# Optimization experiments

Measured on AMD Instinct MI355X. Metric: run time of the kernel, lower is better.

Reference implementation:

```python
import jax, jax.numpy as jnp
import numpy as np

V, E, H, B, T, O = 100000, 300, 512, 512, 64, 2


def setup_inputs() -> dict:
    key = jax.random.key(0)
    ks = jax.random.split(key, 12)
    bound = 1.0 / np.sqrt(H)
    u = lambda k, shape: jax.random.uniform(k, shape, jnp.float32, -bound, bound)
    tokens = jax.random.randint(ks[0], (B, T), 0, V)  # int token ids
    emb = jax.random.normal(ks[1], (V, E), jnp.float32) * 0.05  # pretrained embeddings
    # GRU params stacked over 2 directions: [2, 3H, in], [2, 3H, H], [2, 3H]
    w_ih0 = u(ks[2], (2, 3 * H, E))
    w_hh0 = u(ks[3], (2, 3 * H, H))
    b_ih0 = u(ks[4], (2, 3 * H))
    b_hh0 = u(ks[5], (2, 3 * H))
    w_ih1 = u(ks[6], (2, 3 * H, 2 * H))
    w_hh1 = u(ks[7], (2, 3 * H, H))
    b_ih1 = u(ks[8], (2, 3 * H))
    b_hh1 = u(ks[9], (2, 3 * H))
    fc_w = u(ks[10], (O, 2 * H))
    fc_b = u(ks[11], (O,))
    return dict(tokens=tokens, emb=emb, w_ih0=w_ih0, w_hh0=w_hh0, b_ih0=b_ih0,
                b_hh0=b_hh0, w_ih1=w_ih1, w_hh1=w_hh1, b_ih1=b_ih1, b_hh1=b_hh1,
                fc_w=fc_w, fc_b=fc_b)


def _gru_dir(x, Wih, Whh, bih, bhh):
    # x: [B, T, in] -> [B, T, H]; PyTorch GRU cell math.
    gx = jnp.einsum('bti,gi->btg', x, Wih) + bih  # input gates precomputed [B,T,3H]
    h_units = Whh.shape[1]

    def step(h, g):
        gh = h @ Whh.T + bhh
        xr, xz, xn = jnp.split(g, 3, axis=-1)
        hr, hz, hn = jnp.split(gh, 3, axis=-1)
        r = jax.nn.sigmoid(xr + hr)
        z = jax.nn.sigmoid(xz + hz)
        n = jnp.tanh(xn + r * hn)
        h_new = (1.0 - z) * n + z * h
        return h_new, h_new

    h0 = jnp.zeros((x.shape[0], h_units), x.dtype)
    _, ys = jax.lax.scan(step, h0, jnp.swapaxes(gx, 0, 1))  # scan over time
    return jnp.swapaxes(ys, 0, 1)


def _gru_bidir(x, w_ih, w_hh, b_ih, b_hh):
    fwd = _gru_dir(x, w_ih[0], w_hh[0], b_ih[0], b_hh[0])
    bwd = _gru_dir(x[:, ::-1], w_ih[1], w_hh[1], b_ih[1], b_hh[1])[:, ::-1]
    return jnp.concatenate([fwd, bwd], axis=-1)  # [B, T, 2H]


def reference(tokens, emb, w_ih0, w_hh0, b_ih0, b_hh0, w_ih1, w_hh1, b_ih1,
              b_hh1, fc_w, fc_b):
    x = emb[tokens]                                   # [B, T, E]
    h1 = _gru_bidir(x, w_ih0, w_hh0, b_ih0, b_hh0)    # [B, T, 2H]
    h2 = _gru_bidir(h1, w_ih1, w_hh1, b_ih1, b_hh1)   # [B, T, 2H]
    # dropout output is discarded in the original forward (out = output[:, -1, :])
    last = h2[:, -1, :]                               # [B, 2H]
    return last @ fc_w.T + fc_b                       # [B, O]
```

## Files before the change

kernel.cpp:

```cpp
#include <hip/hip_runtime.h>
#include <stdint.h>


#define NTW 192
#define MTX 2048

typedef _Float16 half8 __attribute__((ext_vector_type(8)));
typedef _Float16 half4_t __attribute__((ext_vector_type(4)));
typedef float float4_t __attribute__((ext_vector_type(4)));

__device__ __forceinline__ void gl_lds16(const void* g, void* l) {
  __builtin_amdgcn_global_load_lds(
      (const __attribute__((address_space(1))) void*)g,
      (__attribute__((address_space(3))) void*)l, 16, 0, 0);
}

__device__ __forceinline__ float sigm_f(float x) { return 1.f / (1.f + __expf(-x)); }
__device__ __forceinline__ float tanh_f(float x) { return 1.f - 2.f / (__expf(2.f * x) + 1.f); }

__global__ void pack_b_kernel(const float* __restrict__ src, _Float16* __restrict__ dst,
                              int K, int KI) {
  int gid = blockIdx.x * 256 + threadIdx.x;
  int l = gid & 63, unit = gid >> 6;
  int nt = unit / KI, ks = unit - nt * KI;
  if (nt >= NTW) return;
  int row = nt * 16 + (l & 15);
  int col0 = ks * 32 + ((l >> 4) << 3);
  half8 v;
#pragma unroll
  for (int j = 0; j < 8; ++j) {
    int c = col0 + j;
    v[j] = (c < K) ? (_Float16)src[(long)row * K + c] : (_Float16)0.f;
  }
  *(half8*)(dst + (long)unit * 512 + l * 8) = v;
}

__global__ void gather_kernel(const int* __restrict__ tokens, const float* __restrict__ emb,
                              _Float16* __restrict__ x0) {
  int gid = blockIdx.x * 256 + threadIdx.x;
  int l = gid & 63, unit = gid >> 6;
  int mt = unit / 10, ks = unit - mt * 10;
  if (mt >= MTX) return;
  int row = mt * 16 + (l & 15);
  const float* e = emb + (long)tokens[row] * 300;
  int col0 = ks * 32 + ((l >> 4) << 3);
  half8 v;
#pragma unroll
  for (int j = 0; j < 8; ++j) {
    int c = col0 + j;
    v[j] = (c < 300) ? (_Float16)e[c] : (_Float16)0.f;
  }
  *(half8*)(x0 + (long)unit * 512 + l * 8) = v;
}

__global__ __launch_bounds__(256) void gemm_bt_kernel(
    const _Float16* __restrict__ A, const _Float16* __restrict__ Bw,
    const float* __restrict__ bias, _Float16* __restrict__ C, int KI) {
  __shared__ _Float16 As[8 * 512];
  __shared__ _Float16 Bs[8 * 512];
  const int bx = blockIdx.x, by = blockIdx.y;
  const int tid = threadIdx.x, w = tid >> 6, l = tid & 63;
  const int wm = w >> 1, wn = w & 1, ln = l & 15;
  const int mt0 = by * 8, nt0 = bx * 8;
  float4_t acc[4][4];
#pragma unroll
  for (int i = 0; i < 4; ++i)
#pragma unroll
    for (int j = 0; j < 4; ++j) acc[i][j] = 0.f;
  for (int it = 0; it < KI; ++it) {
    __syncthreads();
    gl_lds16(A + ((long)(mt0 + w) * KI + it) * 512 + l * 8, As + w * 512 + l * 8);
    gl_lds16(A + ((long)(mt0 + w + 4) * KI + it) * 512 + l * 8, As + (w + 4) * 512 + l * 8);
    gl_lds16(Bw + ((long)(nt0 + w) * KI + it) * 512 + l * 8, Bs + w * 512 + l * 8);
    gl_lds16(Bw + ((long)(nt0 + w + 4) * KI + it) * 512 + l * 8, Bs + (w + 4) * 512 + l * 8);
    __syncthreads();
    half8 af[4], bf[4];
#pragma unroll
    for (int i = 0; i < 4; ++i) af[i] = *(const half8*)(As + (wm * 4 + i) * 512 + l * 8);
#pragma unroll
    for (int j = 0; j < 4; ++j) bf[j] = *(const half8*)(Bs + (wn * 4 + j) * 512 + l * 8);
#pragma unroll
    for (int i = 0; i < 4; ++i)
#pragma unroll
      for (int j = 0; j < 4; ++j)
        acc[i][j] = __builtin_amdgcn_mfma_f32_16x16x32_f16(af[i], bf[j], acc[i][j], 0, 0, 0);
  }
#pragma unroll
  for (int i = 0; i < 4; ++i)
#pragma unroll
    for (int j = 0; j < 4; ++j) {
      int mt = mt0 + wm * 4 + i, ntile = nt0 + wn * 4 + j;
      float bv = bias[ntile * 16 + ln];
      half4_t o;
#pragma unroll
      for (int r = 0; r < 4; ++r) o[r] = (_Float16)(acc[i][j][r] + bv);
      *(half4_t*)(C + ((long)mt * NTW + ntile) * 256 + l * 4) = o;
    }
}

__global__ __launch_bounds__(256, 1) void gru_scan_kernel(
    const _Float16* __restrict__ whh,
    const float* __restrict__ bhh,
    const _Float16* __restrict__ gx,
    _Float16* hbuf, _Float16* ys,
    float* last,
    unsigned int* cnt) {
  __shared__ alignas(16) _Float16 hs[32 * 512];
  __shared__ alignas(16) _Float16 hx[4 * 512];
  const int bid = blockIdx.x;
  const int d = bid >> 7, mtg = (bid >> 3) & 15, ntb = bid & 7;
  const int tid = threadIdx.x, w = tid >> 6, l = tid & 63;
  const int lq = l >> 4, ln = l & 15;
  unsigned int* flags = cnt + (d * 16 + mtg) * 16;
  const int hcol = ntb * 64 + w * 16 + ln;

  half8 bf[3][16];
#pragma unroll
  for (int g = 0; g < 3; ++g) {
    const int tg = d * 96 + g * 32 + ntb * 4 + w;
#pragma unroll
    for (int ks = 0; ks < 16; ++ks)
      bf[g][ks] = *(const half8*)(whh + (long)(tg * 16 + ks) * 512 + l * 8);
  }
  const float bh0 = bhh[d * 1536 + hcol];
  const float bh1 = bhh[d * 1536 + 512 + hcol];
  const float bh2 = bhh[d * 1536 + 1024 + hcol];
  float hreg[2][4] = {{0.f, 0.f, 0.f, 0.f}, {0.f, 0.f, 0.f, 0.f}};
  const int mtr0 = mtg * 2;
  const int ntg0 = d * 96 + ntb * 4 + w;
  const unsigned long long* hb8 = (const unsigned long long*)hbuf;
  unsigned long long* lds64 = (unsigned long long*)hs;

  float xr[2][4], xz[2][4], xn[2][4];
  auto load_gx = [&](int step, float (&vr)[2][4], float (&vz)[2][4], float (&vn)[2][4]) {
    const int t2 = d ? (63 - step) : step;
    const int rm2 = t2 & 15, tq2 = t2 >> 4;
    const int eoff2 = ((rm2 >> 2) * 16 + ln) * 4 + (rm2 & 3);
#pragma unroll
    for (int i = 0; i < 2; ++i)
#pragma unroll
      for (int r = 0; r < 4; ++r) {
        const int b = (mtr0 + i) * 16 + lq * 4 + r;
        const long gbase = ((long)(b * 4 + tq2) * 192 + ntg0) * 256 + eoff2;
        vr[i][r] = (float)gx[gbase];
        vz[i][r] = (float)gx[gbase + 32 * 256];
        vn[i][r] = (float)gx[gbase + 64 * 256];
      }
  };
  load_gx(0, xr, xz, xn);

  for (int s = 0; s < 64; ++s) {
    const int par = s & 1;
    const int t_in = d ? (63 - s) : s;
    const int rm = t_in & 15, tq = t_in >> 4;

    {
      const unsigned long long* src =
          hb8 + (long)(d * 2 + par) * 65536 + (long)mtg * 4096;
#pragma unroll
      for (int rr = 0; rr < 2; ++rr) {
        unsigned long long t0[8];
#pragma unroll
        for (int j = 0; j < 4; ++j) {
          const int f = (rr * 4 + j) * 256 + tid;
          t0[j * 2] = __hip_atomic_load(src + (long)f * 2, __ATOMIC_RELAXED,
                                        __HIP_MEMORY_SCOPE_AGENT);
          t0[j * 2 + 1] = __hip_atomic_load(src + (long)f * 2 + 1, __ATOMIC_RELAXED,
                                            __HIP_MEMORY_SCOPE_AGENT);
        }
#pragma unroll
        for (int j = 0; j < 4; ++j) {
          const int f = (rr * 4 + j) * 256 + tid;
          lds64[f * 2] = t0[j * 2];
          lds64[f * 2 + 1] = t0[j * 2 + 1];
        }
      }
    }
    __syncthreads();

    float4_t acc[3][2];
#pragma unroll
    for (int g = 0; g < 3; ++g) { acc[g][0] = 0.f; acc[g][1] = 0.f; }
#pragma unroll
    for (int kk = 0; kk < 2; ++kk) {
      half8 af[2][8];
#pragma unroll
      for (int i = 0; i < 2; ++i)
#pragma unroll
        for (int k2 = 0; k2 < 8; ++k2)
          af[i][k2] = *(const half8*)(hs + (i * 16 + kk * 8 + k2) * 512 + l * 8);
#pragma unroll
      for (int k2 = 0; k2 < 8; ++k2)
#pragma unroll
        for (int i = 0; i < 2; ++i)
#pragma unroll
          for (int g = 0; g < 3; ++g)
            acc[g][i] = __builtin_amdgcn_mfma_f32_16x16x32_f16(af[i][k2], bf[g][kk * 8 + k2],
                                                               acc[g][i], 0, 0, 0);
    }

#pragma unroll
    for (int i = 0; i < 2; ++i) {
      const int mtile_i = mtr0 + i;
#pragma unroll
      for (int r = 0; r < 4; ++r) {
        const int b = mtile_i * 16 + lq * 4 + r;
        const long gmt = (long)b * 4 + tq;
        const float rg = sigm_f(xr[i][r] + acc[0][i][r] + bh0);
        const float zg = sigm_f(xz[i][r] + acc[1][i][r] + bh1);
        const float ng = tanh_f(xn[i][r] + rg * (acc[2][i][r] + bh2));
        const float hv = (1.f - zg) * ng + zg * hreg[i][r];
        hreg[i][r] = hv;
        hx[(i * 2 + (w >> 1)) * 512 + (((w & 1) * 2 + (ln >> 3)) * 16 + lq * 4 + r) * 8 +
           (ln & 7)] = (_Float16)hv;
        if (ys != nullptr) {
          const int kcol = d * 512 + hcol;
          ys[(gmt * 32 + (kcol >> 5)) * 512 + (((kcol >> 3) & 3) * 16 + rm) * 8 + (kcol & 7)] =
              (_Float16)hv;
        }
        if (last != nullptr && ((d == 0 && s == 63) || (d == 1 && s == 0)))
          last[(long)b * 1024 + d * 512 + hcol] = hv;
      }
    }
    if (s == 63) break;

    __syncthreads();
    {
      const int u = tid >> 6, lw = tid & 63;
      union { half8 h; unsigned long long q[2]; } wb;
      wb.h = *(const half8*)(hx + u * 512 + lw * 8);
      unsigned long long* dst = (unsigned long long*)hbuf +
                                (long)(d * 2 + (par ^ 1)) * 65536 +
                                ((long)((mtg * 2 + (u >> 1)) * 16 + ntb * 2 + (u & 1))) * 128 +
                                lw * 2;
      __hip_atomic_store(dst, wb.q[0], __ATOMIC_RELAXED, __HIP_MEMORY_SCOPE_AGENT);
      __hip_atomic_store(dst + 1, wb.q[1], __ATOMIC_RELAXED, __HIP_MEMORY_SCOPE_AGENT);
    }
    __syncthreads();

    if (tid == 0)
      __hip_atomic_store(flags + ntb, (unsigned int)(s + 1), __ATOMIC_RELAXED,
                         __HIP_MEMORY_SCOPE_AGENT);

    load_gx(s + 1, xr, xz, xn);

    {
      const unsigned int tgt = (unsigned int)(s + 1);
      long guard = 0;
      for (;;) {
        const unsigned int f = __hip_atomic_load(flags + (l & 7), __ATOMIC_RELAXED,
                                                 __HIP_MEMORY_SCOPE_AGENT);
        if (__all((int)(f >= tgt))) break;
        __builtin_amdgcn_s_sleep(1);
        if (++guard > (1L << 24)) break;
      }
      __builtin_amdgcn_fence(__ATOMIC_ACQUIRE, "workgroup");
    }
  }
}

__global__ void fc_kernel(const float* __restrict__ lastb, const float* __restrict__ fw,
                          const float* __restrict__ fb, float* __restrict__ out) {
  const int b = blockIdx.x, l = threadIdx.x;
  const float* x = lastb + (long)b * 1024;
  float a0 = 0.f, a1 = 0.f;
  for (int k = l; k < 1024; k += 64) {
    const float v = x[k];
    a0 += v * fw[k];
    a1 += v * fw[1024 + k];
  }
#pragma unroll
  for (int off = 32; off > 0; off >>= 1) {
    a0 += __shfl_down(a0, off, 64);
    a1 += __shfl_down(a1, off, 64);
  }
  if (l == 0) {
    out[b * 2 + 0] = a0 + fb[0];
    out[b * 2 + 1] = a1 + fb[1];
  }
}

extern "C" void kernel_launch(void* const* d_in, const int* in_sizes, int n_in,
                              void* d_out, int out_size, void* d_ws, size_t ws_size,
                              hipStream_t stream) {
  const int* tokens = (const int*)d_in[0];
  const float* emb = (const float*)d_in[1];
  const float* w_ih0 = (const float*)d_in[2];
  const float* w_hh0 = (const float*)d_in[3];
  const float* b_ih0 = (const float*)d_in[4];
  const float* b_hh0 = (const float*)d_in[5];
  const float* w_ih1 = (const float*)d_in[6];
  const float* w_hh1 = (const float*)d_in[7];
  const float* b_ih1 = (const float*)d_in[8];
  const float* b_hh1 = (const float*)d_in[9];
  const float* fc_w = (const float*)d_in[10];
  const float* fc_b = (const float*)d_in[11];
  float* out = (float*)d_out;

  char* ws = (char*)d_ws;
  size_t off = 0;
  auto alloc = [&](size_t bytes) -> void* {
    void* p = ws + off;
    off += (bytes + 255) & ~(size_t)255;
    return p;
  };
  _Float16* W0f = (_Float16*)alloc(192L * 10 * 512 * 2);
  _Float16* W1f = (_Float16*)alloc(192L * 32 * 512 * 2);
  _Float16* Wh0f = (_Float16*)alloc(192L * 16 * 512 * 2);
  _Float16* Wh1f = (_Float16*)alloc(192L * 16 * 512 * 2);
  _Float16* x0f = (_Float16*)alloc(2048L * 10 * 512 * 2);
  _Float16* x1f = (_Float16*)alloc(2048L * 32 * 512 * 2);
  _Float16* gxb = (_Float16*)alloc(2048L * 192 * 256 * 2);
  char* hz = ws + off;
  _Float16* hbuf = (_Float16*)alloc(4L * 32 * 8192 * 2);
  unsigned int* cnt = (unsigned int*)alloc(4096);
  const size_t hz_bytes = 4L * 32 * 8192 * 2 + 4096;
  float* lastb = (float*)alloc(512L * 1024 * 4);
  if (off > ws_size) return;

  pack_b_kernel<<<dim3(192 * 10 * 64 / 256), 256, 0, stream>>>(w_ih0, W0f, 300, 10);
  pack_b_kernel<<<dim3(192 * 32 * 64 / 256), 256, 0, stream>>>(w_ih1, W1f, 1024, 32);
  pack_b_kernel<<<dim3(192 * 16 * 64 / 256), 256, 0, stream>>>(w_hh0, Wh0f, 512, 16);
  pack_b_kernel<<<dim3(192 * 16 * 64 / 256), 256, 0, stream>>>(w_hh1, Wh1f, 512, 16);
  gather_kernel<<<dim3(2048 * 10 * 64 / 256), 256, 0, stream>>>(tokens, emb, x0f);

  gemm_bt_kernel<<<dim3(24, 256), 256, 0, stream>>>(x0f, W0f, b_ih0, gxb, 10);
  hipMemsetAsync(hz, 0, hz_bytes, stream);
  gru_scan_kernel<<<dim3(256), 256, 0, stream>>>(Wh0f, b_hh0, gxb, hbuf, x1f, nullptr, cnt);

  gemm_bt_kernel<<<dim3(24, 256), 256, 0, stream>>>(x1f, W1f, b_ih1, gxb, 32);
  hipMemsetAsync(hz, 0, hz_bytes, stream);
  gru_scan_kernel<<<dim3(256), 256, 0, stream>>>(Wh1f, b_hh1, gxb, hbuf, nullptr, lastb, cnt);

  fc_kernel<<<dim3(512), 64, 0, stream>>>(lastb, fc_w, fc_b, out);
}
```

Measured before the change: 1.264 ms.

## Split each block's two row tiles into staggered halves with separate flags

Each scan block now handles its two 16-row batch tiles as separate A and B halves, each with its own LDS buffer and completion flag array. Tile A's hidden state is published and flagged before tile B's MFMA and gate math run, so peers waiting on A can proceed earlier. The flag polling also moves to the start of each step, just before the loads, rather than sitting after publication. The aim is to overlap cross-block synchronisation latency with the other tile's compute, at the cost of more barriers and twice as many flag polls per step. It also assumes the flag buffer is sized for 32 row groups per direction instead of 16.

```diff
diff --git a/kernel.cpp b/kernel.cpp
--- a/kernel.cpp
+++ b/kernel.cpp
@@ -105,13 +105,16 @@
     _Float16* hbuf, _Float16* ys,
     float* last,
     unsigned int* cnt) {
-  __shared__ alignas(16) _Float16 hs[32 * 512];
-  __shared__ alignas(16) _Float16 hx[4 * 512];
+  __shared__ alignas(16) _Float16 hsA[16 * 512];
+  __shared__ alignas(16) _Float16 hsB[16 * 512];
+  __shared__ alignas(16) _Float16 hx[2 * 512];
   const int bid = blockIdx.x;
-  const int d = bid >> 7, mtg = (bid >> 3) & 15, ntb = bid & 7;
+  const int d = bid >> 7, mp = (bid >> 3) & 15, ntb = bid & 7;
+  const int rA = mp * 2, rB = rA + 1;
   const int tid = threadIdx.x, w = tid >> 6, l = tid & 63;
   const int lq = l >> 4, ln = l & 15;
-  unsigned int* flags = cnt + (d * 16 + mtg) * 16;
+  unsigned int* flagsA = cnt + (d * 32 + rA) * 16;
+  unsigned int* flagsB = cnt + (d * 32 + rB) * 16;
   const int hcol = ntb * 64 + w * 16 + ln;
 
   half8 bf[3][16];
@@ -125,137 +128,166 @@
   const float bh0 = bhh[d * 1536 + hcol];
   const float bh1 = bhh[d * 1536 + 512 + hcol];
   const float bh2 = bhh[d * 1536 + 1024 + hcol];
-  float hreg[2][4] = {{0.f, 0.f, 0.f, 0.f}, {0.f, 0.f, 0.f, 0.f}};
-  const int mtr0 = mtg * 2;
+  float hrA[4] = {0.f, 0.f, 0.f, 0.f};
+  float hrB[4] = {0.f, 0.f, 0.f, 0.f};
   const int ntg0 = d * 96 + ntb * 4 + w;
   const unsigned long long* hb8 = (const unsigned long long*)hbuf;
-  unsigned long long* lds64 = (unsigned long long*)hs;
-
-  float xr[2][4], xz[2][4], xn[2][4];
-  auto load_gx = [&](int step, float (&vr)[2][4], float (&vz)[2][4], float (&vn)[2][4]) {
+  unsigned long long* hb8w = (unsigned long long*)hbuf;
+  unsigned long long* lA64 = (unsigned long long*)hsA;
+  unsigned long long* lB64 = (unsigned long long*)hsB;
+  const unsigned long long* hx64 = (const unsigned long long*)hx;
+
+  float xrA[4], xzA[4], xnA[4], xrB[4], xzB[4], xnB[4];
+  auto load_gx = [&](int step, int rc, float (&vr)[4], float (&vz)[4], float (&vn)[4]) {
     const int t2 = d ? (63 - step) : step;
     const int rm2 = t2 & 15, tq2 = t2 >> 4;
     const int eoff2 = ((rm2 >> 2) * 16 + ln) * 4 + (rm2 & 3);
 #pragma unroll
-    for (int i = 0; i < 2; ++i)
-#pragma unroll
-      for (int r = 0; r < 4; ++r) {
-        const int b = (mtr0 + i) * 16 + lq * 4 + r;
-        const long gbase = ((long)(b * 4 + tq2) * 192 + ntg0) * 256 + eoff2;
-        vr[i][r] = (float)gx[gbase];
-        vz[i][r] = (float)gx[gbase + 32 * 256];
-        vn[i][r] = (float)gx[gbase + 64 * 256];
-      }
+    for (int r = 0; r < 4; ++r) {
+      const int b = rc * 16 + lq * 4 + r;
+      const long gbase = ((long)(b * 4 + tq2) * 192 + ntg0) * 256 + eoff2;
+      vr[r] = (float)gx[gbase];
+      vz[r] = (float)gx[gbase + 32 * 256];
+      vn[r] = (float)gx[gbase + 64 * 256];
+    }
   };
-  load_gx(0, xr, xz, xn);
+  load_gx(0, rA, xrA, xzA, xnA);
+  load_gx(0, rB, xrB, xzB, xnB);
+
+  auto poll = [&](unsigned int* flags, unsigned int tgt) {
+    long guard = 0;
+    for (;;) {
+      const unsigned int f = __hip_atomic_load(flags + (l & 7), __ATOMIC_RELAXED,
+                                               __HIP_MEMORY_SCOPE_AGENT);
+      if (__all((int)(f >= tgt))) break;
+      __builtin_amdgcn_s_sleep(1);
+      if (++guard > (1L << 24)) break;
+    }
+  };
 
   for (int s = 0; s < 64; ++s) {
     const int par = s & 1;
     const int t_in = d ? (63 - s) : s;
     const int rm = t_in & 15, tq = t_in >> 4;
-
+    const unsigned long long* src = hb8 + (long)(d * 2 + par) * 65536;
+
+    poll(flagsA, (unsigned int)s);
+    poll(flagsB, (unsigned int)s);
+    __builtin_amdgcn_fence(__ATOMIC_ACQUIRE, "workgroup");
+    unsigned long long ta[8], tb[8];
+#pragma unroll
+    for (int j = 0; j < 8; ++j)
+      ta[j] = __hip_atomic_load(src + (long)rA * 2048 + j * 256 + tid, __ATOMIC_RELAXED,
+                                __HIP_MEMORY_SCOPE_AGENT);
+#pragma unroll
+    for (int j = 0; j < 8; ++j)
+      tb[j] = __hip_atomic_load(src + (long)rB * 2048 + j * 256 + tid, __ATOMIC_RELAXED,
+                                __HIP_MEMORY_SCOPE_AGENT);
+#pragma unroll
+    for (int j = 0; j < 8; ++j) lA64[j * 256 + tid] = ta[j];
+    __syncthreads();
+
+    float4_t accA[3];
+    accA[0] = 0.f; accA[1] = 0.f; accA[2] = 0.f;
+#pragma unroll
+    for (int kk = 0; kk < 2; ++kk) {
+      half8 af[8];
+#pragma unroll
+      for (int k2 = 0; k2 < 8; ++k2)
+        af[k2] = *(const half8*)(hsA + (kk * 8 + k2) * 512 + l * 8);
+#pragma unroll
+      for (int k2 = 0; k2 < 8; ++k2)
+#pragma unroll
+        for (int g = 0; g < 3; ++g)
+          accA[g] = __builtin_amdgcn_mfma_f32_16x16x32_f16(af[k2], bf[g][kk * 8 + k2],
+                                                           accA[g], 0, 0, 0);
+    }
+#pragma unroll
+    for (int j = 0; j < 8; ++j) lB64[j * 256 + tid] = tb[j];
+
+#pragma unroll
+    for (int r = 0; r < 4; ++r) {
+      const int b = rA * 16 + lq * 4 + r;
+      const long gmt = (long)b * 4 + tq;
+      const float rg = sigm_f(xrA[r] + accA[0][r] + bh0);
+      const float zg = sigm_f(xzA[r] + accA[1][r] + bh1);
+      const float ng = tanh_f(xnA[r] + rg * (accA[2][r] + bh2));
+      const float hv = (1.f - zg) * ng + zg * hrA[r];
+      hrA[r] = hv;
+      hx[(w >> 1) * 512 + (((w & 1) * 2 + (ln >> 3)) * 16 + lq * 4 + r) * 8 + (ln & 7)] =
+          (_Float16)hv;
+      if (ys != nullptr) {
+        const int kcol = d * 512 + hcol;
+        ys[(gmt * 32 + (kcol >> 5)) * 512 + (((kcol >> 3) & 3) * 16 + rm) * 8 + (kcol & 7)] =
+            (_Float16)hv;
+      }
+      if (last != nullptr && ((d == 0 && s == 63) || (d == 1 && s == 0)))
+        last[(long)b * 1024 + d * 512 + hcol] = hv;
+    }
+    __syncthreads();
+
+    if (s < 63) {
+      const unsigned long long qa = hx64[tid];
+      unsigned long long* dst = hb8w + (long)(d * 2 + (par ^ 1)) * 65536 +
+                                (long)rA * 2048 + (ntb * 2 + (tid >> 7)) * 128 + (tid & 127);
+      __hip_atomic_store(dst, qa, __ATOMIC_RELAXED, __HIP_MEMORY_SCOPE_AGENT);
+    }
+
+    float4_t accB[3];
+    accB[0] = 0.f; accB[1] = 0.f; accB[2] = 0.f;
+#pragma unroll
+    for (int kk = 0; kk < 2; ++kk) {
+      half8 af[8];
+#pragma unroll
+      for (int k2 = 0; k2 < 8; ++k2)
+        af[k2] = *(const half8*)(hsB + (kk * 8 + k2) * 512 + l * 8);
+#pragma unroll
+      for (int k2 = 0; k2 < 8; ++k2)
+#pragma unroll
+        for (int g = 0; g < 3; ++g)
+          accB[g] = __builtin_amdgcn_mfma_f32_16x16x32_f16(af[k2], bf[g][kk * 8 + k2],
+                                                           accB[g], 0, 0, 0);
+    }
+    __syncthreads();
+    if (tid == 0 && s < 63)
+      __hip_atomic_store(flagsA + ntb, (unsigned int)(s + 1), __ATOMIC_RELAXED,
+                         __HIP_MEMORY_SCOPE_AGENT);
+
+#pragma unroll
+    for (int r = 0; r < 4; ++r) {
+      const int b = rB * 16 + lq * 4 + r;
+      const long gmt = (long)b * 4 + tq;
+      const float rg = sigm_f(xrB[r] + accB[0][r] + bh0);
+      const float zg = sigm_f(xzB[r] + accB[1][r] + bh1);
+      const float ng = tanh_f(xnB[r] + rg * (accB[2][r] + bh2));
+      const float hv = (1.f - zg) * ng + zg * hrB[r];
+      hrB[r] = hv;
+      hx[(w >> 1) * 512 + (((w & 1) * 2 + (ln >> 3)) * 16 + lq * 4 + r) * 8 + (ln & 7)] =
+          (_Float16)hv;
+      if (ys != nullptr) {
+        const int kcol = d * 512 + hcol;
+        ys[(gmt * 32 + (kcol >> 5)) * 512 + (((kcol >> 3) & 3) * 16 + rm) * 8 + (kcol & 7)] =
+            (_Float16)hv;
+      }
+      if (last != nullptr && ((d == 0 && s == 63) || (d == 1 && s == 0)))
+        last[(long)b * 1024 + d * 512 + hcol] = hv;
+    }
+    if (s == 63) break;
+
+    __syncthreads();
     {
-      const unsigned long long* src =
-          hb8 + (long)(d * 2 + par) * 65536 + (long)mtg * 4096;
-#pragma unroll
-      for (int rr = 0; rr < 2; ++rr) {
-        unsigned long long t0[8];
-#pragma unroll
-        for (int j = 0; j < 4; ++j) {
-          const int f = (rr * 4 + j) * 256 + tid;
-          t0[j * 2] = __hip_atomic_load(src + (long)f * 2, __ATOMIC_RELAXED,
-                                        __HIP_MEMORY_SCOPE_AGENT);
-          t0[j * 2 + 1] = __hip_atomic_load(src + (long)f * 2 + 1, __ATOMIC_RELAXED,
-                                            __HIP_MEMORY_SCOPE_AGENT);
-        }
-#pragma unroll
-        for (int j = 0; j < 4; ++j) {
-          const int f = (rr * 4 + j) * 256 + tid;
-          lds64[f * 2] = t0[j * 2];
-          lds64[f * 2 + 1] = t0[j * 2 + 1];
-        }
-      }
-    }
-    __syncthreads();
-
-    float4_t acc[3][2];
-#pragma unroll
-    for (int g = 0; g < 3; ++g) { acc[g][0] = 0.f; acc[g][1] = 0.f; }
-#pragma unroll
-    for (int kk = 0; kk < 2; ++kk) {
-      half8 af[2][8];
-#pragma unroll
-      for (int i = 0; i < 2; ++i)
-#pragma unroll
-        for (int k2 = 0; k2 < 8; ++k2)
-          af[i][k2] = *(const half8*)(hs + (i * 16 + kk * 8 + k2) * 512 + l * 8);
-#pragma unroll
-      for (int k2 = 0; k2 < 8; ++k2)
-#pragma unroll
-        for (int i = 0; i < 2; ++i)
-#pragma unroll
-          for (int g = 0; g < 3; ++g)
-            acc[g][i] = __builtin_amdgcn_mfma_f32_16x16x32_f16(af[i][k2], bf[g][kk * 8 + k2],
-                                                               acc[g][i], 0, 0, 0);
-    }
-
-#pragma unroll
-    for (int i = 0; i < 2; ++i) {
-      const int mtile_i = mtr0 + i;
-#pragma unroll
-      for (int r = 0; r < 4; ++r) {
-        const int b = mtile_i * 16 + lq * 4 + r;
-        const long gmt = (long)b * 4 + tq;
-        const float rg = sigm_f(xr[i][r] + acc[0][i][r] + bh0);
-        const float zg = sigm_f(xz[i][r] + acc[1][i][r] + bh1);
-        const float ng = tanh_f(xn[i][r] + rg * (acc[2][i][r] + bh2));
-        const float hv = (1.f - zg) * ng + zg * hreg[i][r];
-        hreg[i][r] = hv;
-        hx[(i * 2 + (w >> 1)) * 512 + (((w & 1) * 2 + (ln >> 3)) * 16 + lq * 4 + r) * 8 +
-           (ln & 7)] = (_Float16)hv;
-        if (ys != nullptr) {
-          const int kcol = d * 512 + hcol;
-          ys[(gmt * 32 + (kcol >> 5)) * 512 + (((kcol >> 3) & 3) * 16 + rm) * 8 + (kcol & 7)] =
-              (_Float16)hv;
-        }
-        if (last != nullptr && ((d == 0 && s == 63) || (d == 1 && s == 0)))
-          last[(long)b * 1024 + d * 512 + hcol] = hv;
-      }
-    }
-    if (s == 63) break;
-
-    __syncthreads();
-    {
-      const int u = tid >> 6, lw = tid & 63;
-      union { half8 h; unsigned long long q[2]; } wb;
-      wb.h = *(const half8*)(hx + u * 512 + lw * 8);
-      unsigned long long* dst = (unsigned long long*)hbuf +
-                                (long)(d * 2 + (par ^ 1)) * 65536 +
-                                ((long)((mtg * 2 + (u >> 1)) * 16 + ntb * 2 + (u & 1))) * 128 +
-                                lw * 2;
-      __hip_atomic_store(dst, wb.q[0], __ATOMIC_RELAXED, __HIP_MEMORY_SCOPE_AGENT);
-      __hip_atomic_store(dst + 1, wb.q[1], __ATOMIC_RELAXED, __HIP_MEMORY_SCOPE_AGENT);
-    }
-    __syncthreads();
-
+      const unsigned long long qb = hx64[tid];
+      unsigned long long* dst = hb8w + (long)(d * 2 + (par ^ 1)) * 65536 +
+                                (long)rB * 2048 + (ntb * 2 + (tid >> 7)) * 128 + (tid & 127);
+      __hip_atomic_store(dst, qb, __ATOMIC_RELAXED, __HIP_MEMORY_SCOPE_AGENT);
+    }
+    __syncthreads();
     if (tid == 0)
-      __hip_atomic_store(flags + ntb, (unsigned int)(s + 1), __ATOMIC_RELAXED,
+      __hip_atomic_store(flagsB + ntb, (unsigned int)(s + 1), __ATOMIC_RELAXED,
                          __HIP_MEMORY_SCOPE_AGENT);
 
-    load_gx(s + 1, xr, xz, xn);
-
-    {
-      const unsigned int tgt = (unsigned int)(s + 1);
-      long guard = 0;
-      for (;;) {
-        const unsigned int f = __hip_atomic_load(flags + (l & 7), __ATOMIC_RELAXED,
-                                                 __HIP_MEMORY_SCOPE_AGENT);
-        if (__all((int)(f >= tgt))) break;
-        __builtin_amdgcn_s_sleep(1);
-        if (++guard > (1L << 24)) break;
-      }
-      __builtin_amdgcn_fence(__ATOMIC_ACQUIRE, "workgroup");
-    }
+    load_gx(s + 1, rA, xrA, xzA, xnA);
+    load_gx(s + 1, rB, xrB, xzB, xnB);
   }
 }
 
```

Result: faster. 1.218 ms (-3.6%).
